# Kernel optimization log

Measured on AMD Instinct MI355X. Metric: run time of the kernel, lower is better.

The kernel has to match this reference:

```python
import jax, jax.numpy as jnp
import numpy as np

B, S, D, H, HD = 1, 2048, 1024, 16, 64
GH = 64            # GammaGate hidden dim
FFN_H = int(D * 4 * 2 / 3)
CTX = 512          # omega-rule context window c
LAM = 0.999        # base exponential decay

def _rms(x, w, eps=1e-6):
    return x * jax.lax.rsqrt(jnp.mean(x * x, axis=-1, keepdims=True) + eps) * w

def _rope(q, k):
    hd = q.shape[-1]; s = q.shape[2]
    inv = 1.0 / (10000.0 ** (jnp.arange(0, hd, 2, dtype=jnp.float32) / hd))
    fr = jnp.arange(s, dtype=jnp.float32)[:, None] * inv[None, :]
    cos = jnp.concatenate([jnp.cos(fr), jnp.cos(fr)], -1)
    sin = jnp.concatenate([jnp.sin(fr), jnp.sin(fr)], -1)
    rot = lambda x: jnp.concatenate([-x[..., hd // 2:], x[..., :hd // 2]], -1)
    return q * cos + rot(q) * sin, k * cos + rot(k) * sin

def setup_inputs() -> dict:
    key = jax.random.key(0)
    ks = jax.random.split(key, 10)
    n = lambda i, sh, s=0.02: jax.random.normal(ks[i], sh, jnp.float32) * s
    return dict(
        x=jax.random.normal(ks[0], (B, S, D), jnp.float32),
        norm1_w=jnp.ones((D,), jnp.float32),
        norm2_w=jnp.ones((D,), jnp.float32),
        w_qkv=n(1, (D, 3 * D)),
        q_norm_w=jnp.ones((HD,), jnp.float32),
        k_norm_w=jnp.ones((HD,), jnp.float32),
        gamma_w1=n(2, (D, GH)),
        gamma_w2=n(3, (GH, 1)),
        m_persist=n(4, (H, HD, HD)),
        memory_gate=jnp.array([-3.0], jnp.float32),
        w_o=n(5, (D, D), 0.02 / 2 ** 0.5),
        ffn_w1=n(6, (D, FFN_H)),
        ffn_w3=n(7, (D, FFN_H)),
        ffn_w2=n(8, (FFN_H, D)),
    )

def reference(x, norm1_w, norm2_w, w_qkv, q_norm_w, k_norm_w, gamma_w1, gamma_w2,
              m_persist, memory_gate, w_o, ffn_w1, ffn_w3, ffn_w2):
    b, s, d = x.shape
    h = _rms(x, norm1_w)
    qkv = h @ w_qkv
    q, k, v = jnp.split(qkv, 3, axis=-1)
    rs = lambda t: t.reshape(b, s, H, HD).transpose(0, 2, 1, 3)   # (b,h,s,hd)
    q, k, v = rs(q), rs(k), rs(v)
    q = _rms(q, q_norm_w); k = _rms(k, k_norm_w)                  # qk_norm
    q, k = _rope(q, k)
    # input-dependent gamma gate: Linear->SiLU->Linear->Sigmoid
    gamma = jax.nn.sigmoid(jax.nn.silu(h @ gamma_w1) @ gamma_w2)  # (b,s,1)
    # Omega-rule memory: Q'_t = (M_p q_t + sum_i w_{t,i} k_i (k_i . q_t)) / (1 + sum_i w_{t,i})
    ti = jnp.arange(s)
    delta = ti[:, None] - ti[None, :]
    wmask = (delta >= 0) & (delta < CTX)
    decay = jnp.where(wmask, LAM ** delta.astype(jnp.float32), 0.0)      # (t,i)
    w = decay[None, None] * gamma[:, None, None, :, 0]                   # (b,1,t,i)
    norm = 1.0 + jnp.sum(w, axis=-1)                                     # (b,1,t)
    scores = jnp.einsum('bhtd,bhid->bhti', q, k)
    contrib = jnp.einsum('bhti,bhid->bhtd', w * scores, k)
    persist = jnp.einsum('hde,bhte->bhtd', m_persist, q)
    qp = (persist + contrib) / norm[..., None]
    gate = jax.nn.sigmoid(memory_gate)[0]
    q = (1.0 - gate) * q + gate * qp
    # causal attention
    aw = jnp.einsum('bhtd,bhid->bhti', q, k) * (HD ** -0.5)
    causal = ti[:, None] >= ti[None, :]
    aw = jnp.where(causal[None, None], aw, -jnp.inf)
    aw = jax.nn.softmax(aw, axis=-1)
    ao = jnp.einsum('bhti,bhid->bhtd', aw, v).transpose(0, 2, 1, 3).reshape(b, s, d)
    x = x + ao @ w_o
    h2 = _rms(x, norm2_w)
    x = x + (jax.nn.silu(h2 @ ffn_w1) * (h2 @ ffn_w3)) @ ffn_w2   # SwiGLU
    return x
```

## Files before the change

### kernel.cpp

```cpp
#include <hip/hip_runtime.h>
#include <hip/hip_bf16.h>

#define S_LEN 2048
#define D_DIM 1024
#define H_NUM 16
#define HD_DIM 64
#define GH_DIM 64
#define FFN_H 2730
#define FFNP  2816
#define CTX_W 512
#define L2LAM -0.00144341687f
#define QBLK 64
#define KBLK 64
#define ALDK 76
#define QSCALE 0.1803368801111731f

typedef unsigned short u16;
typedef __attribute__((ext_vector_type(8))) short bf16x8_t;
typedef __attribute__((ext_vector_type(4))) float f32x4_t;

__device__ inline float wave_sum(float v) {
    for (int off = 32; off; off >>= 1) v += __shfl_xor(v, off);
    return v;
}
__device__ inline u16 f2bf(float f) {
    unsigned r;
    asm("v_cvt_pk_bf16_f32 %0, %1, %2" : "=v"(r) : "v"(f), "v"(f));
    return (u16)r;
}
__device__ inline unsigned f2bf2(float lo, float hi) {
    unsigned r;
    asm("v_cvt_pk_bf16_f32 %0, %1, %2" : "=v"(r) : "v"(lo), "v"(hi));
    return r;
}
__device__ inline float bf2f(u16 u) {
    return __uint_as_float(((unsigned int)u) << 16);
}
__device__ inline void gload16(const void* g, void* l) {
    __builtin_amdgcn_global_load_lds(
        (const __attribute__((address_space(1))) void*)g,
        (__attribute__((address_space(3))) void*)l, 16, 0, 0);
}

__global__ __launch_bounds__(256) void rmsnorm_kernel(
    const float* __restrict__ in, const float* __restrict__ w,
    u16* __restrict__ out)
{
    __shared__ float wsum[4];
    int row = blockIdx.x;
    int tid = threadIdx.x, lane = tid & 63, wv = tid >> 6;
    const float4* ir = reinterpret_cast<const float4*>(in + (size_t)row * D_DIM);
    float4 v = ir[tid];
    float ss = v.x*v.x + v.y*v.y + v.z*v.z + v.w*v.w;
    ss = wave_sum(ss);
    if (lane == 0) wsum[wv] = ss;
    __syncthreads();
    float tot = wsum[0] + wsum[1] + wsum[2] + wsum[3];
    float scale = rsqrtf(tot / (float)D_DIM + 1e-6f);
    const float4* wr = reinterpret_cast<const float4*>(w);
    float4 wv4 = wr[tid];
    uint2 o;
    o.x = f2bf2(v.x * scale * wv4.x, v.y * scale * wv4.y);
    o.y = f2bf2(v.z * scale * wv4.z, v.w * scale * wv4.w);
    *reinterpret_cast<uint2*>(out + (size_t)row * D_DIM + tid * 4) = o;
}

__global__ __launch_bounds__(256) void prep_kernel(
    const float* __restrict__ w_qkv, const float* __restrict__ gw1f,
    u16* __restrict__ wqT, u16* __restrict__ gw1T,
    const float* __restrict__ x, const float* __restrict__ norm1_w,
    u16* __restrict__ h_bf)
{
    __shared__ float tile[64][65];
    __shared__ float wsum[4];
    int b = blockIdx.x;
    int tid = threadIdx.x;
    if (b < 784) {
        const float* src; u16* dst;
        int srcK, srcN, Kp, nbx;
        if (b < 768) {           src = w_qkv; dst = wqT;  srcK = 1024; srcN = 3072; Kp = 1024; nbx = 48; }
        else         { b -= 768; src = gw1f;  dst = gw1T; srcK = 1024; srcN = 64;   Kp = 1024; nbx = 1; }
        int n0 = (b % nbx) * 64, k0 = (b / nbx) * 64;
        int tx = tid & 15, ty = tid >> 4;
        bool interior = (k0 + 63 < srcK) && (n0 + 63 < srcN);
        #pragma unroll
        for (int p = 0; p < 4; ++p) {
            int kk = p * 16 + ty;
            int r = k0 + kk;
            int cb = n0 + tx * 4;
            float4 v;
            if (interior) {
                v = *(const float4*)(src + (size_t)r * srcN + cb);
            } else {
                v.x = (r < srcK && cb     < srcN) ? src[(size_t)r * srcN + cb]     : 0.f;
                v.y = (r < srcK && cb + 1 < srcN) ? src[(size_t)r * srcN + cb + 1] : 0.f;
                v.z = (r < srcK && cb + 2 < srcN) ? src[(size_t)r * srcN + cb + 2] : 0.f;
                v.w = (r < srcK && cb + 3 < srcN) ? src[(size_t)r * srcN + cb + 3] : 0.f;
            }
            tile[kk][tx*4+0] = v.x; tile[kk][tx*4+1] = v.y;
            tile[kk][tx*4+2] = v.z; tile[kk][tx*4+3] = v.w;
        }
        __syncthreads();
        int wx = tid & 7, wy = tid >> 3;
        #pragma unroll
        for (int p = 0; p < 2; ++p) {
            int nn = p * 32 + wy;
            int ks = wx * 8;
            uint4 o;
            o.x = f2bf2(tile[ks+0][nn], tile[ks+1][nn]);
            o.y = f2bf2(tile[ks+2][nn], tile[ks+3][nn]);
            o.z = f2bf2(tile[ks+4][nn], tile[ks+5][nn]);
            o.w = f2bf2(tile[ks+6][nn], tile[ks+7][nn]);
            *(uint4*)(dst + (size_t)(n0 + nn) * Kp + k0 + ks) = o;
        }
    } else {
        int row = b - 784;
        int lane = tid & 63, wv = tid >> 6;
        const float4* ir = reinterpret_cast<const float4*>(x + (size_t)row * D_DIM);
        float4 v = ir[tid];
        float ss = v.x*v.x + v.y*v.y + v.z*v.z + v.w*v.w;
        ss = wave_sum(ss);
        if (lane == 0) wsum[wv] = ss;
        __syncthreads();
        float tot = wsum[0] + wsum[1] + wsum[2] + wsum[3];
        float scale = rsqrtf(tot / (float)D_DIM + 1e-6f);
        const float4* wr = reinterpret_cast<const float4*>(norm1_w);
        float4 wv4 = wr[tid];
        uint2 o;
        o.x = f2bf2(v.x * scale * wv4.x, v.y * scale * wv4.y);
        o.y = f2bf2(v.z * scale * wv4.z, v.w * scale * wv4.w);
        *reinterpret_cast<uint2*>(h_bf + (size_t)row * D_DIM + tid * 4) = o;
    }
}

__global__ __launch_bounds__(256) void split_gamma_kernel(
    const u16* __restrict__ qkv, const float* __restrict__ qw,
    const float* __restrict__ kw, float* __restrict__ qhp,
    u16* __restrict__ khp, u16* __restrict__ khT, u16* __restrict__ vhT,
    const u16* __restrict__ h_bf, const u16* __restrict__ gw1T,
    const float* __restrict__ w2, float* __restrict__ gamma)
{
    __shared__ char smem[2 * 64 * ALDK * 2];
    int tid = threadIdx.x;
    int b = blockIdx.x;
    if (b < 512) {
        u16 (*tk)[ALDK] = (u16(*)[ALDK])smem;
        u16 (*tv)[ALDK] = (u16(*)[ALDK])(smem + 64 * ALDK * 2);
        int w = tid >> 6, d = tid & 63;
        int h = b >> 5;
        int s0 = (b & 31) * 64;
        float qwv = qw[d], kwv = kw[d];
        int j = d & 31;
        float inv = expf(-(float)j * (9.2103403719761836f / 32.0f));
        float sgn = (d < 32) ? -1.f : 1.f;
        for (int i = 0; i < 16; ++i) {
            int sl = w * 16 + i;
            int s = s0 + sl;
            size_t base = (size_t)s * (3 * D_DIM) + h * HD_DIM + d;
            float qv = bf2f(qkv[base]);
            float kv = bf2f(qkv[base + D_DIM]);
            u16  vv = qkv[base + 2 * D_DIM];
            float sq = wave_sum(qv * qv);
            float qn = qv * rsqrtf(sq / (float)HD_DIM + 1e-6f) * qwv;
            float sk = wave_sum(kv * kv);
            float kn = kv * rsqrtf(sk / (float)HD_DIM + 1e-6f) * kwv;
            float ang = (float)s * inv;
            float cs = cosf(ang), sn = sinf(ang);
            float qp = __shfl_xor(qn, 32);
            float kp = __shfl_xor(kn, 32);
            float qo = qn * cs + sgn * qp * sn;
            float ko = kn * cs + sgn * kp * sn;
            size_t ob = ((size_t)h * S_LEN + s) * HD_DIM + d;
            u16 kb = f2bf(ko);
            qhp[ob] = qo;
            khp[ob] = kb;
            tk[sl][d] = kb;
            tv[sl][d] = vv;
        }
        __syncthreads();
        int r = tid >> 2, cc = (tid & 3) * 16;
        union { u16 u[16]; bf16x8_t v[2]; } ok, ov;
        #pragma unroll
        for (int e = 0; e < 16; ++e) {
            int ksrc = (e & 3) * 16 + (tid & 3) * 4 + (e >> 2);
            ok.u[e] = tk[ksrc][r]; ov.u[e] = tv[ksrc][r];
        }
        u16* kd = khT + ((size_t)h * HD_DIM + r) * S_LEN + s0 + cc;
        u16* vd = vhT + ((size_t)h * HD_DIM + r) * S_LEN + s0 + cc;
        *(bf16x8_t*)kd       = ok.v[0];
        *(bf16x8_t*)(kd + 8) = ok.v[1];
        *(bf16x8_t*)vd       = ov.v[0];
        *(bf16x8_t*)(vd + 8) = ov.v[1];
    } else {
        u16* As = (u16*)smem;
        u16* Bs = (u16*)(smem + 8192);
        float (*red)[64] = (float(*)[64])(smem + 16384);
        int lane = tid & 63, wid = tid >> 6;
        int wr = wid >> 1, wc = wid & 1;
        int row0 = (b - 512) * 64;
        int l8 = lane >> 3, l7 = lane & 7;
        f32x4_t acc[2][2];
        #pragma unroll
        for (int i = 0; i < 2; ++i)
            #pragma unroll
            for (int j2 = 0; j2 < 2; ++j2) acc[i][j2] = (f32x4_t)0.f;
        int fr = lane & 15, fo = (lane >> 4) * 8;
        for (int k0 = 0; k0 < D_DIM; k0 += 64) {
            #pragma unroll
            for (int i = 0; i < 2; ++i) {
                int ch = wid * 2 + i;
                const u16* ga = h_bf + (size_t)(row0 + ch * 8 + l8) * D_DIM + k0 + l7 * 8;
                gload16(ga, &As[ch * 512]);
                const u16* gb = gw1T + (size_t)(ch * 8 + l8) * D_DIM + k0 + l7 * 8;
                gload16(gb, &Bs[ch * 512]);
            }
            __syncthreads();
            __builtin_amdgcn_s_setprio(1);
            #pragma unroll
            for (int khf = 0; khf < 2; ++khf) {
                bf16x8_t bfrag[2];
                #pragma unroll
                for (int ni = 0; ni < 2; ++ni)
                    bfrag[ni] = *(const bf16x8_t*)&Bs[(wc * 32 + ni * 16 + fr) * 64 + khf * 32 + fo];
                #pragma unroll
                for (int mi = 0; mi < 2; ++mi) {
                    bf16x8_t af = *(const bf16x8_t*)&As[(wr * 32 + mi * 16 + fr) * 64 + khf * 32 + fo];
                    #pragma unroll
                    for (int ni = 0; ni < 2; ++ni)
                        acc[mi][ni] = __builtin_amdgcn_mfma_f32_16x16x32_bf16(
                            af, bfrag[ni], acc[mi][ni], 0, 0, 0);
                }
            }
            __builtin_amdgcn_s_setprio(0);
            __syncthreads();
        }
        int dr = (lane >> 4) * 4, dc = lane & 15;
        float w2v0 = w2[wc * 32 + dc];
        float w2v1 = w2[wc * 32 + 16 + dc];
        #pragma unroll
        for (int mi = 0; mi < 2; ++mi) {
            #pragma unroll
            for (int j2 = 0; j2 < 4; ++j2) {
                float v0 = acc[mi][0][j2];
                float v1 = acc[mi][1][j2];
                float t = v0 / (1.f + __expf(-v0)) * w2v0
                        + v1 / (1.f + __expf(-v1)) * w2v1;
                t += __shfl_xor(t, 1);
                t += __shfl_xor(t, 2);
                t += __shfl_xor(t, 4);
                t += __shfl_xor(t, 8);
                if (dc == 0) red[wc][wr * 32 + mi * 16 + dr + j2] = t;
            }
        }
        __syncthreads();
        if (tid < 64) {
            float g = red[0][tid] + red[1][tid];
            gamma[row0 + tid] = 1.f / (1.f + __expf(-g));
        }
    }
}

template<int BM, int MODE>
__global__ __launch_bounds__(256) void gemm_bb_kernel(
    const u16* __restrict__ A, const u16* __restrict__ B,
    u16* __restrict__ Cb, int M, int N, int K)
{
    constexpr int MREP = BM / 32;
    constexpr int ACH  = BM / 32;
    __shared__ u16 As[BM * 64];
    __shared__ u16 Bs[128 * 64];
    int tid = threadIdx.x, lane = tid & 63, wid = tid >> 6;
    int wr = wid >> 1, wc = wid & 1;
    int row0 = blockIdx.y * BM, col0 = blockIdx.x * 128;
    int l8 = lane >> 3, l7 = lane & 7;
    f32x4_t acc[MREP][4];
    #pragma unroll
    for (int i = 0; i < MREP; ++i)
        #pragma unroll
        for (int j = 0; j < 4; ++j) acc[i][j] = (f32x4_t)0.f;

    int fr = lane & 15, fo = (lane >> 4) * 8;
    for (int k0 = 0; k0 < K; k0 += 64) {
        #pragma unroll
        for (int i = 0; i < ACH; ++i) {
            int ch = wid * ACH + i;
            const u16* ga = A + (size_t)(row0 + ch * 8 + l8) * K + k0 + l7 * 8;
            gload16(ga, &As[ch * 512]);
        }
        #pragma unroll
        for (int i = 0; i < 4; ++i) {
            int ch = wid * 4 + i;
            const u16* gb = B + (size_t)(col0 + ch * 8 + l8) * K + k0 + l7 * 8;
            gload16(gb, &Bs[ch * 512]);
        }
        __syncthreads();
        __builtin_amdgcn_s_setprio(1);
        #pragma unroll
        for (int khf = 0; khf < 2; ++khf) {
            bf16x8_t bfrag[4];
            #pragma unroll
            for (int ni = 0; ni < 4; ++ni)
                bfrag[ni] = *(const bf16x8_t*)&Bs[(wc * 64 + ni * 16 + fr) * 64 + khf * 32 + fo];
            #pragma unroll
            for (int mi = 0; mi < MREP; ++mi) {
                bf16x8_t af = *(const bf16x8_t*)&As[(wr * (BM / 2) + mi * 16 + fr) * 64 + khf * 32 + fo];
                #pragma unroll
                for (int ni = 0; ni < 4; ++ni)
                    acc[mi][ni] = __builtin_amdgcn_mfma_f32_16x16x32_bf16(
                        af, bfrag[ni], acc[mi][ni], 0, 0, 0);
            }
        }
        __builtin_amdgcn_s_setprio(0);
        __syncthreads();
    }
    int dr = (lane >> 4) * 4, dc = lane & 15;
    #pragma unroll
    for (int mi = 0; mi < MREP; ++mi) {
        int gr = row0 + wr * (BM / 2) + mi * 16 + dr;
        #pragma unroll
        for (int ni = 0; ni < 4; ++ni) {
            int gc = col0 + wc * 64 + ni * 16 + dc;
            #pragma unroll
            for (int j = 0; j < 4; ++j) {
                float v = acc[mi][ni][j];
                if (MODE == 1) {
                    Cb[(size_t)(gr + j) * N + gc] = f2bf(v);
                } else {
                    float partner = __shfl_xor(v, 1);
                    float a1 = (dc & 1) ? partner : v;
                    float a3 = (dc & 1) ? v : partner;
                    float rr = a1 / (1.f + __expf(-a1)) * a3;
                    if (!(dc & 1))
                        Cb[(size_t)(gr + j) * (N >> 1) + (gc >> 1)] = f2bf(rr);
                }
            }
        }
    }
}

__global__ __launch_bounds__(256) void gemm64_kernel(
    const u16* __restrict__ A, const u16* __restrict__ B,
    const float* __restrict__ res, float* __restrict__ Cf,
    int M, int N, int K)
{
    __shared__ u16 As[64 * 64];
    __shared__ u16 Bs[64 * 64];
    int tid = threadIdx.x, lane = tid & 63, wid = tid >> 6;
    int wr = wid >> 1, wc = wid & 1;
    int row0 = blockIdx.y * 64, col0 = blockIdx.x * 64;
    int l8 = lane >> 3, l7 = lane & 7;
    f32x4_t acc[2][2];
    #pragma unroll
    for (int i = 0; i < 2; ++i)
        #pragma unroll
        for (int j = 0; j < 2; ++j) acc[i][j] = (f32x4_t)0.f;
    int fr = lane & 15, fo = (lane >> 4) * 8;
    for (int k0 = 0; k0 < K; k0 += 64) {
        #pragma unroll
        for (int i = 0; i < 2; ++i) {
            int ch = wid * 2 + i;
            const u16* ga = A + (size_t)(row0 + ch * 8 + l8) * K + k0 + l7 * 8;
            gload16(ga, &As[ch * 512]);
            const u16* gb = B + (size_t)(col0 + ch * 8 + l8) * K + k0 + l7 * 8;
            gload16(gb, &Bs[ch * 512]);
        }
        __syncthreads();
        __builtin_amdgcn_s_setprio(1);
        #pragma unroll
        for (int khf = 0; khf < 2; ++khf) {
            bf16x8_t bfrag[2];
            #pragma unroll
            for (int ni = 0; ni < 2; ++ni)
                bfrag[ni] = *(const bf16x8_t*)&Bs[(wc * 32 + ni * 16 + fr) * 64 + khf * 32 + fo];
            #pragma unroll
            for (int mi = 0; mi < 2; ++mi) {
                bf16x8_t af = *(const bf16x8_t*)&As[(wr * 32 + mi * 16 + fr) * 64 + khf * 32 + fo];
                #pragma unroll
                for (int ni = 0; ni < 2; ++ni)
                    acc[mi][ni] = __builtin_amdgcn_mfma_f32_16x16x32_bf16(
                        af, bfrag[ni], acc[mi][ni], 0, 0, 0);
            }
        }
        __builtin_amdgcn_s_setprio(0);
        __syncthreads();
    }
    int dr = (lane >> 4) * 4, dc = lane & 15;
    #pragma unroll
    for (int mi = 0; mi < 2; ++mi) {
        int gr = row0 + wr * 32 + mi * 16 + dr;
        #pragma unroll
        for (int ni = 0; ni < 2; ++ni) {
            int gc = col0 + wc * 32 + ni * 16 + dc;
            #pragma unroll
            for (int j = 0; j < 4; ++j) {
                size_t off = (size_t)(gr + j) * N + gc;
                Cf[off] = acc[mi][ni][j] + res[off];
            }
        }
    }
}

__global__ __launch_bounds__(512) void fused_omega_attn_kernel(
    const float* __restrict__ qhp, const u16* __restrict__ khp,
    const u16* __restrict__ khT, const u16* __restrict__ vhT,
    const float* __restrict__ gammab, const float* __restrict__ mp,
    const float* __restrict__ mg, u16* __restrict__ ao,
    const float* __restrict__ w_o, const float* __restrict__ w1f,
    const float* __restrict__ w3f, const float* __restrict__ w2f,
    u16* __restrict__ woT, u16* __restrict__ w13T, u16* __restrict__ w2T)
{
    __shared__ u16 Ks[2][KBLK][ALDK];
    __shared__ u16 Xt[2][KBLK][ALDK];
    __shared__ u16 Ps[QBLK][ALDK];
    __shared__ float colfL[CTX_W + KBLK];
    __shared__ float redS[2][QBLK];
    const int tid = threadIdx.x, lane = tid & 63, wid = tid >> 6;
    const int b = blockIdx.x;

    if (b >= 512) {
        int b2 = b - 512;
        const float* src; u16* dst;
        int srcK, srcN, Kp, rowOff, rowMul, nbx;
        if (b2 < 256)       {             src = w_o; dst = woT;  srcK = 1024; srcN = 1024; Kp = 1024; rowOff = 0; rowMul = 1; nbx = 16; }
        else if (b2 < 960)  { b2 -= 256;  src = w1f; dst = w13T; srcK = 1024; srcN = 2730; Kp = 1024; rowOff = 0; rowMul = 2; nbx = 44; }
        else if (b2 < 1664) { b2 -= 960;  src = w3f; dst = w13T; srcK = 1024; srcN = 2730; Kp = 1024; rowOff = 1; rowMul = 2; nbx = 44; }
        else                { b2 -= 1664; src = w2f; dst = w2T;  srcK = 2730; srcN = 1024; Kp = 2816; rowOff = 0; rowMul = 1; nbx = 16; }
        int n0 = (b2 % nbx) * 64, k0 = (b2 / nbx) * 64;
        float* tile = (float*)&Ks[0][0][0];
        int tx = tid & 15, ty = tid >> 4;
        bool interior = (k0 + 63 < srcK) && (n0 + 63 < srcN);
        #pragma unroll
        for (int p = 0; p < 2; ++p) {
            int kk = p * 32 + ty;
            int r = k0 + kk;
            int cb = n0 + tx * 4;
            float4 v;
            if (interior) {
                v = *(const float4*)(src + (size_t)r * srcN + cb);
            } else {
                v.x = (r < srcK && cb     < srcN) ? src[(size_t)r * srcN + cb]     : 0.f;
                v.y = (r < srcK && cb + 1 < srcN) ? src[(size_t)r * srcN + cb + 1] : 0.f;
                v.z = (r < srcK && cb + 2 < srcN) ? src[(size_t)r * srcN + cb + 2] : 0.f;
                v.w = (r < srcK && cb + 3 < srcN) ? src[(size_t)r * srcN + cb + 3] : 0.f;
            }
            tile[kk * 65 + tx*4+0] = v.x; tile[kk * 65 + tx*4+1] = v.y;
            tile[kk * 65 + tx*4+2] = v.z; tile[kk * 65 + tx*4+3] = v.w;
        }
        __syncthreads();
        int wx = tid & 7, wy = tid >> 3;
        int nn = wy, ks = wx * 8;
        uint4 o;
        o.x = f2bf2(tile[(ks+0) * 65 + nn], tile[(ks+1) * 65 + nn]);
        o.y = f2bf2(tile[(ks+2) * 65 + nn], tile[(ks+3) * 65 + nn]);
        o.z = f2bf2(tile[(ks+4) * 65 + nn], tile[(ks+5) * 65 + nn]);
        o.w = f2bf2(tile[(ks+6) * 65 + nn], tile[(ks+7) * 65 + nn]);
        *(uint4*)(dst + (size_t)(rowOff + (size_t)(n0 + nn) * rowMul) * Kp + k0 + ks) = o;
        return;
    }

    const int wq = wid & 3;
    const int nh = wid >> 2;
    const int hi = (b >> 8) & 1;
    const int h = ((b & 7) << 1) + hi;
    const int s5 = (b >> 3) & 31;
    const int qt = hi ? (31 - s5) : s5;
    const int q0 = qt * QBLK;
    const int fr = lane & 15, g4 = lane >> 4;
    const int fko = g4 * 8;
    const int c = fr, rg = g4;
    const int si = tid >> 3, sdb = (tid & 7) * 8;
    const size_t hS = (size_t)h * S_LEN;
    const size_t hD = (size_t)h * HD_DIM;

    int rowt[4]; float rowf[4];
    #pragma unroll
    for (int j = 0; j < 4; ++j) {
        rowt[j] = q0 + wq * 16 + rg * 4 + j;
        rowf[j] = exp2f((float)(wq * 16 + rg * 4 + j) * L2LAM);
    }
    bf16x8_t qf[2];
    {
        const float* qrow = qhp + (hS + q0 + wq * 16 + fr) * HD_DIM;
        #pragma unroll
        for (int u = 0; u < 2; ++u) {
            float4 a = *(const float4*)(qrow + u * 32 + fko);
            float4 bq = *(const float4*)(qrow + u * 32 + fko + 4);
            bf16x8_t f;
            f[0]=f2bf(a.x); f[1]=f2bf(a.y); f[2]=f2bf(a.z); f[3]=f2bf(a.w);
            f[4]=f2bf(bq.x); f[5]=f2bf(bq.y); f[6]=f2bf(bq.z); f[7]=f2bf(bq.w);
            qf[u] = f;
        }
    }
    float qold[2][4];
    #pragma unroll
    for (int nn = 0; nn < 2; ++nn)
        #pragma unroll
        for (int j = 0; j < 4; ++j)
            qold[nn][j] = qhp[(hS + rowt[j]) * HD_DIM + (nh * 2 + nn) * 16 + c];

    f32x4_t accc[2];
    accc[0] = (f32x4_t)0.f; accc[1] = (f32x4_t)0.f;
    float wsum[4] = {0.f, 0.f, 0.f, 0.f};
    const int kt0 = (q0 > (CTX_W - 1)) ? (q0 - (CTX_W - 1)) / KBLK : 0;
    const int i0 = kt0 * KBLK;
    const int nwin = (qt + 1) * KBLK - i0;
    for (int idx = tid; idx < nwin; idx += 512) {
        int icol = i0 + idx;
        colfL[idx] = exp2f((float)(q0 - icol) * L2LAM) * gammab[icol];
    }
    {
        const u16* gk = khp + (hS + kt0 * KBLK + si) * HD_DIM + sdb;
        const u16* gx = khT + (hD + si) * S_LEN + kt0 * KBLK + sdb;
        *(bf16x8_t*)&Ks[0][si][sdb] = *(const bf16x8_t*)gk;
        *(bf16x8_t*)&Xt[0][si][sdb] = *(const bf16x8_t*)gx;
    }
    __syncthreads();
    int cur = 0;
    for (int kt = kt0; kt <= qt; ++kt) {
        const int k0 = kt * KBLK;
        const bool hn = (kt < qt);
        bf16x8_t nk0, nx0;
        if (hn) {
            const u16* gk = khp + (hS + k0 + KBLK + si) * HD_DIM + sdb;
            const u16* gx = khT + (hD + si) * S_LEN + k0 + KBLK + sdb;
            nk0 = *(const bf16x8_t*)gk;
            nx0 = *(const bf16x8_t*)gx;
        }
        f32x4_t s[2];
        s[0] = (f32x4_t)0.f; s[1] = (f32x4_t)0.f;
        __builtin_amdgcn_s_setprio(1);
        #pragma unroll
        for (int u = 0; u < 2; ++u)
            #pragma unroll
            for (int nn = 0; nn < 2; ++nn) {
                bf16x8_t kb = *(const bf16x8_t*)&Ks[cur][(nh * 2 + nn) * 16 + fr][u * 32 + fko];
                s[nn] = __builtin_amdgcn_mfma_f32_16x16x32_bf16(qf[u], kb, s[nn], 0, 0, 0);
            }
        __builtin_amdgcn_s_setprio(0);
        const bool boundary = (kt == kt0) || (kt == qt);
        float colf[2];
        #pragma unroll
        for (int nn = 0; nn < 2; ++nn)
            colf[nn] = colfL[k0 - i0 + (nh * 2 + nn) * 16 + c];
        #pragma unroll
        for (int j = 0; j < 4; ++j) {
            float pv[2];
            #pragma unroll
            for (int nn = 0; nn < 2; ++nn) {
                float w;
                if (boundary) {
                    int delta = rowt[j] - (k0 + (nh * 2 + nn) * 16 + c);
                    w = (delta >= 0 && delta < CTX_W) ? rowf[j] * colf[nn] : 0.f;
                } else {
                    w = rowf[j] * colf[nn];
                }
                wsum[j] += w;
                pv[nn] = w * s[nn][j];
            }
            *(unsigned*)&Ps[wq * 16 + rg * 4 + j][c * 4 + nh * 2] = f2bf2(pv[0], pv[1]);
        }
        __syncthreads();
        __builtin_amdgcn_s_setprio(1);
        #pragma unroll
        for (int u = 0; u < 2; ++u) {
            bf16x8_t pa = *(const bf16x8_t*)&Ps[wq * 16 + fr][u * 32 + fko];
            #pragma unroll
            for (int nn = 0; nn < 2; ++nn) {
                bf16x8_t kb = *(const bf16x8_t*)&Xt[cur][(nh * 2 + nn) * 16 + fr][u * 32 + fko];
                accc[nn] = __builtin_amdgcn_mfma_f32_16x16x32_bf16(pa, kb, accc[nn], 0, 0, 0);
            }
        }
        __builtin_amdgcn_s_setprio(0);
        if (hn) {
            int nxt = cur ^ 1;
            *(bf16x8_t*)&Ks[nxt][si][sdb] = nk0;
            *(bf16x8_t*)&Xt[nxt][si][sdb] = nx0;
        }
        __syncthreads();
        cur ^= 1;
    }
    f32x4_t pacc[2];
    pacc[0] = (f32x4_t)0.f; pacc[1] = (f32x4_t)0.f;
    const float* mph = mp + hD * HD_DIM;
    #pragma unroll
    for (int u = 0; u < 2; ++u)
        #pragma unroll
        for (int nn = 0; nn < 2; ++nn) {
            const float* br = mph + (size_t)((nh * 2 + nn) * 16 + fr) * HD_DIM + u * 32 + fko;
            float4 a = *(const float4*)br;
            float4 bq = *(const float4*)(br + 4);
            bf16x8_t f;
            f[0]=f2bf(a.x); f[1]=f2bf(a.y); f[2]=f2bf(a.z); f[3]=f2bf(a.w);
            f[4]=f2bf(bq.x); f[5]=f2bf(bq.y); f[6]=f2bf(bq.z); f[7]=f2bf(bq.w);
            pacc[nn] = __builtin_amdgcn_mfma_f32_16x16x32_bf16(qf[u], f, pacc[nn], 0, 0, 0);
        }
    #pragma unroll
    for (int j = 0; j < 4; ++j) {
        wsum[j] += __shfl_xor(wsum[j], 1);
        wsum[j] += __shfl_xor(wsum[j], 2);
        wsum[j] += __shfl_xor(wsum[j], 4);
        wsum[j] += __shfl_xor(wsum[j], 8);
    }
    if (fr == 0) {
        #pragma unroll
        for (int j = 0; j < 4; ++j)
            redS[nh][wq * 16 + rg * 4 + j] = wsum[j];
    }
    __syncthreads();
    float wtot[4];
    #pragma unroll
    for (int j = 0; j < 4; ++j)
        wtot[j] = redS[0][wq * 16 + rg * 4 + j] + redS[1][wq * 16 + rg * 4 + j];
    float gate = 1.f / (1.f + __expf(-mg[0]));
    float keep = 1.f - gate;
    #pragma unroll
    for (int nn = 0; nn < 2; ++nn) {
        #pragma unroll
        for (int j = 0; j < 4; ++j) {
            float qn = keep * qold[nn][j] + gate * (pacc[nn][j] + accc[nn][j]) / (1.f + wtot[j]);
            Ps[wq * 16 + rg * 4 + j][(nh * 2 + nn) * 16 + c] = f2bf(qn * QSCALE);
        }
    }
    __syncthreads();
    bf16x8_t qf2[2];
    #pragma unroll
    for (int u = 0; u < 2; ++u)
        qf2[u] = *(const bf16x8_t*)&Ps[wq * 16 + fr][u * 32 + fko];

    f32x4_t acco[2];
    acco[0] = (f32x4_t)0.f; acco[1] = (f32x4_t)0.f;
    float l_run[4] = {0.f, 0.f, 0.f, 0.f};
    {
        const u16* gk = khp + (hS + si) * HD_DIM + sdb;
        const u16* gv = vhT + (hD + si) * S_LEN + sdb;
        *(bf16x8_t*)&Ks[0][si][sdb] = *(const bf16x8_t*)gk;
        *(bf16x8_t*)&Xt[0][si][sdb] = *(const bf16x8_t*)gv;
    }
    __syncthreads();
    cur = 0;
    for (int kt = 0; kt <= qt; ++kt) {
        const int k0 = kt * KBLK;
        const bool hn = (kt < qt);
        bf16x8_t nk0, nv0;
        if (hn) {
            const u16* gk = khp + (hS + k0 + KBLK + si) * HD_DIM + sdb;
            const u16* gv = vhT + (hD + si) * S_LEN + k0 + KBLK + sdb;
            nk0 = *(const bf16x8_t*)gk;
            nv0 = *(const bf16x8_t*)gv;
        }
        f32x4_t s[2];
        s[0] = (f32x4_t)0.f; s[1] = (f32x4_t)0.f;
        __builtin_amdgcn_s_setprio(1);
        #pragma unroll
        for (int u = 0; u < 2; ++u)
            #pragma unroll
            for (int nn = 0; nn < 2; ++nn) {
                bf16x8_t kb = *(const bf16x8_t*)&Ks[cur][(nh * 2 + nn) * 16 + fr][u * 32 + fko];
                s[nn] = __builtin_amdgcn_mfma_f32_16x16x32_bf16(qf2[u], kb, s[nn], 0, 0, 0);
            }
        __builtin_amdgcn_s_setprio(0);
        if (kt == qt) {
            #pragma unroll
            for (int nn = 0; nn < 2; ++nn) {
                int icol = k0 + (nh * 2 + nn) * 16 + c;
                #pragma unroll
                for (int j = 0; j < 4; ++j)
                    if (icol > rowt[j]) s[nn][j] = -1e30f;
            }
        }
        #pragma unroll
        for (int j = 0; j < 4; ++j) {
            float p0 = exp2f(s[0][j]);
            float p1 = exp2f(s[1][j]);
            l_run[j] += p0 + p1;
            *(unsigned*)&Ps[wq * 16 + rg * 4 + j][c * 4 + nh * 2] = f2bf2(p0, p1);
        }
        __syncthreads();
        __builtin_amdgcn_s_setprio(1);
        #pragma unroll
        for (int u = 0; u < 2; ++u) {
            bf16x8_t pa = *(const bf16x8_t*)&Ps[wq * 16 + fr][u * 32 + fko];
            #pragma unroll
            for (int nn = 0; nn < 2; ++nn) {
                bf16x8_t vb = *(const bf16x8_t*)&Xt[cur][(nh * 2 + nn) * 16 + fr][u * 32 + fko];
                acco[nn] = __builtin_amdgcn_mfma_f32_16x16x32_bf16(pa, vb, acco[nn], 0, 0, 0);
            }
        }
        __builtin_amdgcn_s_setprio(0);
        if (hn) {
            int nxt = cur ^ 1;
            *(bf16x8_t*)&Ks[nxt][si][sdb] = nk0;
            *(bf16x8_t*)&Xt[nxt][si][sdb] = nv0;
        }
        __syncthreads();
        cur ^= 1;
    }
    #pragma unroll
    for (int j = 0; j < 4; ++j) {
        l_run[j] += __shfl_xor(l_run[j], 1);
        l_run[j] += __shfl_xor(l_run[j], 2);
        l_run[j] += __shfl_xor(l_run[j], 4);
        l_run[j] += __shfl_xor(l_run[j], 8);
    }
    if (fr == 0) {
        #pragma unroll
        for (int j = 0; j < 4; ++j)
            redS[nh][wq * 16 + rg * 4 + j] = l_run[j];
    }
    __syncthreads();
    #pragma unroll
    for (int j = 0; j < 4; ++j)
        l_run[j] = redS[0][wq * 16 + rg * 4 + j] + redS[1][wq * 16 + rg * 4 + j];
    #pragma unroll
    for (int nn = 0; nn < 2; ++nn) {
        #pragma unroll
        for (int j = 0; j < 4; ++j) {
            float o = acco[nn][j] / l_run[j];
            ao[(size_t)rowt[j] * D_DIM + h * HD_DIM + (nh * 2 + nn) * 16 + c] = f2bf(o);
        }
    }
}

extern "C" void kernel_launch(void* const* d_in, const int* in_sizes, int n_in,
                              void* d_out, int out_size, void* d_ws, size_t ws_size,
                              hipStream_t stream) {
    const float* x         = (const float*)d_in[0];
    const float* norm1_w   = (const float*)d_in[1];
    const float* norm2_w   = (const float*)d_in[2];
    const float* w_qkv     = (const float*)d_in[3];
    const float* q_norm_w  = (const float*)d_in[4];
    const float* k_norm_w  = (const float*)d_in[5];
    const float* gamma_w1  = (const float*)d_in[6];
    const float* gamma_w2  = (const float*)d_in[7];
    const float* m_persist = (const float*)d_in[8];
    const float* mem_gate  = (const float*)d_in[9];
    const float* w_o       = (const float*)d_in[10];
    const float* ffn_w1    = (const float*)d_in[11];
    const float* ffn_w3    = (const float*)d_in[12];
    const float* ffn_w2    = (const float*)d_in[13];
    float* out = (float*)d_out;
    char* ws = (char*)d_ws;

    const size_t MB = 1024 * 1024;
    u16*   h_bf   = (u16*)(ws);
    u16*   wqT    = (u16*)(ws + 4 * MB);
    u16*   woT    = (u16*)(ws + 10 * MB);
    u16*   w13T   = (u16*)(ws + 12 * MB);
    u16*   w2T    = (u16*)(ws + 23 * MB);
    u16*   qkv_bf = (u16*)(ws + 29884416);
    u16*   ao_bf  = (u16*)(ws + 38273024);
    float* qh     = (float*)(ws + 42467328);
    u16*   kh     = (u16*)(ws + 50855936);
    u16*   khT_s  = (u16*)(ws + 50855936 + 4 * MB);
    float* gammab = (float*)(ws + 59244544);
    u16*   vhT_s  = (u16*)(ws + 59244544 + 65536);
    u16*   gw1T   = (u16*)(ws + 63504384);
    u16*   mid_bf = (u16*)(ws + 29884416);

    hipLaunchKernelGGL(prep_kernel, dim3(784 + S_LEN), dim3(256), 0, stream,
                       w_qkv, gamma_w1, wqT, gw1T, x, norm1_w, h_bf);

    hipLaunchKernelGGL((gemm_bb_kernel<64, 1>), dim3(24, 32), dim3(256), 0, stream,
                       h_bf, wqT, qkv_bf, S_LEN, 3 * D_DIM, D_DIM);
    hipLaunchKernelGGL(split_gamma_kernel, dim3(512 + 32), dim3(256), 0, stream,
                       qkv_bf, q_norm_w, k_norm_w, qh, kh, khT_s, vhT_s,
                       h_bf, gw1T, gamma_w2, gammab);
    hipLaunchKernelGGL(fused_omega_attn_kernel, dim3(512 + 2368), dim3(512), 0, stream,
                       qh, kh, khT_s, vhT_s, gammab, m_persist, mem_gate, ao_bf,
                       w_o, ffn_w1, ffn_w3, ffn_w2, woT, w13T, w2T);
    hipLaunchKernelGGL(gemm64_kernel, dim3(16, 32), dim3(256), 0, stream,
                       ao_bf, woT, x, out, S_LEN, D_DIM, D_DIM);
    hipLaunchKernelGGL(rmsnorm_kernel, dim3(S_LEN), dim3(256), 0, stream,
                       out, norm2_w, h_bf);
    hipLaunchKernelGGL((gemm_bb_kernel<128, 2>), dim3(44, 16), dim3(256), 0, stream,
                       h_bf, w13T, mid_bf, S_LEN, 2 * FFNP, D_DIM);
    hipLaunchKernelGGL(gemm64_kernel, dim3(16, 32), dim3(256), 0, stream,
                       mid_bf, w2T, out, out, S_LEN, D_DIM, FFNP);
}
```

Baseline: 195.8 us.

## Triple-buffer K/V tiles and double-buffer P to drop per-iteration barrier

Both the omega-memory loop and the causal attention loop now keep three K/X (or K/V) LDS buffers, prefetching two tiles ahead, and two P staging buffers alternating on kt parity. This makes the trailing __syncthreads in each iteration unnecessary, leaving one barrier per tile instead of two. LDS usage grows to about 80 KB per block, which may limit how many blocks fit on a CU.

```diff
diff --git a/kernel.cpp b/kernel.cpp
--- a/kernel.cpp
+++ b/kernel.cpp
@@ -409,9 +409,9 @@
     const float* __restrict__ w3f, const float* __restrict__ w2f,
     u16* __restrict__ woT, u16* __restrict__ w13T, u16* __restrict__ w2T)
 {
-    __shared__ u16 Ks[2][KBLK][ALDK];
-    __shared__ u16 Xt[2][KBLK][ALDK];
-    __shared__ u16 Ps[QBLK][ALDK];
+    __shared__ u16 Ks[3][KBLK][ALDK];
+    __shared__ u16 Xt[3][KBLK][ALDK];
+    __shared__ u16 Ps[2][QBLK][ALDK];
     __shared__ float colfL[CTX_W + KBLK];
     __shared__ float redS[2][QBLK];
     const int tid = threadIdx.x, lane = tid & 63, wid = tid >> 6;
@@ -513,16 +513,20 @@
         const u16* gx = khT + (hD + si) * S_LEN + kt0 * KBLK + sdb;
         *(bf16x8_t*)&Ks[0][si][sdb] = *(const bf16x8_t*)gk;
         *(bf16x8_t*)&Xt[0][si][sdb] = *(const bf16x8_t*)gx;
+        if (kt0 < qt) {
+            *(bf16x8_t*)&Ks[1][si][sdb] = *(const bf16x8_t*)(gk + (size_t)KBLK * HD_DIM);
+            *(bf16x8_t*)&Xt[1][si][sdb] = *(const bf16x8_t*)(gx + KBLK);
+        }
     }
     __syncthreads();
     int cur = 0;
     for (int kt = kt0; kt <= qt; ++kt) {
         const int k0 = kt * KBLK;
-        const bool hn = (kt < qt);
+        const bool pf = (kt + 2 <= qt);
         bf16x8_t nk0, nx0;
-        if (hn) {
-            const u16* gk = khp + (hS + k0 + KBLK + si) * HD_DIM + sdb;
-            const u16* gx = khT + (hD + si) * S_LEN + k0 + KBLK + sdb;
+        if (pf) {
+            const u16* gk = khp + (hS + k0 + 2 * KBLK + si) * HD_DIM + sdb;
+            const u16* gx = khT + (hD + si) * S_LEN + k0 + 2 * KBLK + sdb;
             nk0 = *(const bf16x8_t*)gk;
             nx0 = *(const bf16x8_t*)gx;
         }
@@ -557,13 +561,13 @@
                 wsum[j] += w;
                 pv[nn] = w * s[nn][j];
             }
-            *(unsigned*)&Ps[wq * 16 + rg * 4 + j][c * 4 + nh * 2] = f2bf2(pv[0], pv[1]);
+            *(unsigned*)&Ps[kt & 1][wq * 16 + rg * 4 + j][c * 4 + nh * 2] = f2bf2(pv[0], pv[1]);
         }
         __syncthreads();
         __builtin_amdgcn_s_setprio(1);
         #pragma unroll
         for (int u = 0; u < 2; ++u) {
-            bf16x8_t pa = *(const bf16x8_t*)&Ps[wq * 16 + fr][u * 32 + fko];
+            bf16x8_t pa = *(const bf16x8_t*)&Ps[kt & 1][wq * 16 + fr][u * 32 + fko];
             #pragma unroll
             for (int nn = 0; nn < 2; ++nn) {
                 bf16x8_t kb = *(const bf16x8_t*)&Xt[cur][(nh * 2 + nn) * 16 + fr][u * 32 + fko];
@@ -571,13 +575,12 @@
             }
         }
         __builtin_amdgcn_s_setprio(0);
-        if (hn) {
-            int nxt = cur ^ 1;
-            *(bf16x8_t*)&Ks[nxt][si][sdb] = nk0;
-            *(bf16x8_t*)&Xt[nxt][si][sdb] = nx0;
-        }
-        __syncthreads();
-        cur ^= 1;
+        if (pf) {
+            int w = cur - 1; if (w < 0) w += 3;
+            *(bf16x8_t*)&Ks[w][si][sdb] = nk0;
+            *(bf16x8_t*)&Xt[w][si][sdb] = nx0;
+        }
+        cur = (cur == 2) ? 0 : cur + 1;
     }
     f32x4_t pacc[2];
     pacc[0] = (f32x4_t)0.f; pacc[1] = (f32x4_t)0.f;
@@ -618,14 +621,14 @@
         #pragma unroll
         for (int j = 0; j < 4; ++j) {
             float qn = keep * qold[nn][j] + gate * (pacc[nn][j] + accc[nn][j]) / (1.f + wtot[j]);
-            Ps[wq * 16 + rg * 4 + j][(nh * 2 + nn) * 16 + c] = f2bf(qn * QSCALE);
+            Ps[0][wq * 16 + rg * 4 + j][(nh * 2 + nn) * 16 + c] = f2bf(qn * QSCALE);
         }
     }
     __syncthreads();
     bf16x8_t qf2[2];
     #pragma unroll
     for (int u = 0; u < 2; ++u)
-        qf2[u] = *(const bf16x8_t*)&Ps[wq * 16 + fr][u * 32 + fko];
+        qf2[u] = *(const bf16x8_t*)&Ps[0][wq * 16 + fr][u * 32 + fko];
 
     f32x4_t acco[2];
     acco[0] = (f32x4_t)0.f; acco[1] = (f32x4_t)0.f;
@@ -635,16 +638,20 @@
         const u16* gv = vhT + (hD + si) * S_LEN + sdb;
         *(bf16x8_t*)&Ks[0][si][sdb] = *(const bf16x8_t*)gk;
         *(bf16x8_t*)&Xt[0][si][sdb] = *(const bf16x8_t*)gv;
+        if (qt > 0) {
+            *(bf16x8_t*)&Ks[1][si][sdb] = *(const bf16x8_t*)(gk + (size_t)KBLK * HD_DIM);
+            *(bf16x8_t*)&Xt[1][si][sdb] = *(const bf16x8_t*)(gv + KBLK);
+        }
     }
     __syncthreads();
     cur = 0;
     for (int kt = 0; kt <= qt; ++kt) {
         const int k0 = kt * KBLK;
-        const bool hn = (kt < qt);
+        const bool pf = (kt + 2 <= qt);
         bf16x8_t nk0, nv0;
-        if (hn) {
-            const u16* gk = khp + (hS + k0 + KBLK + si) * HD_DIM + sdb;
-            const u16* gv = vhT + (hD + si) * S_LEN + k0 + KBLK + sdb;
+        if (pf) {
+            const u16* gk = khp + (hS + k0 + 2 * KBLK + si) * HD_DIM + sdb;
+            const u16* gv = vhT + (hD + si) * S_LEN + k0 + 2 * KBLK + sdb;
             nk0 = *(const bf16x8_t*)gk;
             nv0 = *(const bf16x8_t*)gv;
         }
@@ -673,13 +680,13 @@
             float p0 = exp2f(s[0][j]);
             float p1 = exp2f(s[1][j]);
             l_run[j] += p0 + p1;
-            *(unsigned*)&Ps[wq * 16 + rg * 4 + j][c * 4 + nh * 2] = f2bf2(p0, p1);
+            *(unsigned*)&Ps[kt & 1][wq * 16 + rg * 4 + j][c * 4 + nh * 2] = f2bf2(p0, p1);
         }
         __syncthreads();
         __builtin_amdgcn_s_setprio(1);
         #pragma unroll
         for (int u = 0; u < 2; ++u) {
-            bf16x8_t pa = *(const bf16x8_t*)&Ps[wq * 16 + fr][u * 32 + fko];
+            bf16x8_t pa = *(const bf16x8_t*)&Ps[kt & 1][wq * 16 + fr][u * 32 + fko];
             #pragma unroll
             for (int nn = 0; nn < 2; ++nn) {
                 bf16x8_t vb = *(const bf16x8_t*)&Xt[cur][(nh * 2 + nn) * 16 + fr][u * 32 + fko];
@@ -687,13 +694,12 @@
             }
         }
         __builtin_amdgcn_s_setprio(0);
-        if (hn) {
-            int nxt = cur ^ 1;
-            *(bf16x8_t*)&Ks[nxt][si][sdb] = nk0;
-            *(bf16x8_t*)&Xt[nxt][si][sdb] = nv0;
-        }
-        __syncthreads();
-        cur ^= 1;
+        if (pf) {
+            int w = cur - 1; if (w < 0) w += 3;
+            *(bf16x8_t*)&Ks[w][si][sdb] = nk0;
+            *(bf16x8_t*)&Xt[w][si][sdb] = nv0;
+        }
+        cur = (cur == 2) ? 0 : cur + 1;
     }
     #pragma unroll
     for (int j = 0; j < 4; ++j) {
```

After: 194.6 us. No clear change (-0.6%).
